# Kernel tuning notes

Hardware: AMD Instinct MI355X
Metric: run time of the kernel (lower is better)

## Reference

```python
import jax, jax.numpy as jnp
import numpy as np

T, B, D_IN, D_H, D_OUT = 16, 8192, 512, 1024, 256


def setup_inputs() -> dict:
    key = jax.random.key(0)
    ks = jax.random.split(key, 4)
    # He-style scaled init to keep activations sane
    x = jax.random.normal(ks[0], (B, D_IN), dtype=jnp.float32)
    W1 = jax.random.normal(ks[1], (T, D_IN, D_H), dtype=jnp.float32) / np.sqrt(D_IN)
    b1 = jnp.zeros((T, D_H), dtype=jnp.float32)
    W2 = jax.random.normal(ks[2], (T, D_H, D_H), dtype=jnp.float32) / np.sqrt(D_H)
    b2 = jnp.zeros((T, D_H), dtype=jnp.float32)
    W3 = jax.random.normal(ks[3], (T, D_H, D_OUT), dtype=jnp.float32) / np.sqrt(D_H)
    b3 = jnp.zeros((T, D_OUT), dtype=jnp.float32)
    return {"x": x, "W1": W1, "b1": b1, "W2": W2, "b2": b2, "W3": W3, "b3": b3}


def reference(x, W1, b1, W2, b2, W3, b3):
    # Batched over the tree dimension t: one grouped GEMM per layer instead of
    # a Python loop over trees.
    h = jax.nn.relu(jnp.einsum('bi,tih->tbh', x, W1) + b1[:, None, :])   # [T,B,H]
    h = jax.nn.relu(jnp.einsum('tbh,thk->tbk', h, W2) + b2[:, None, :])  # [T,B,H]
    out = jnp.einsum('tbh,tho->tbo', h, W3) + b3[:, None, :]             # [T,B,O]
    return jnp.mean(out, axis=0)                                          # [B,O]
```

## Files before the change

kernel.cpp:

```cpp
#include <hip/hip_runtime.h>
#include <hip/hip_bf16.h>
#include <stdint.h>

#define T_TREES 16
#define B_ROWS  8192
#define DIN     512
#define DH      1024
#define DOUT    256

typedef unsigned short u16;
typedef __attribute__((ext_vector_type(8))) short short8;
typedef __attribute__((ext_vector_type(16))) float floatx16;

__device__ __forceinline__ u16 f2bf(float f) {
    union { float f; uint32_t u; } v; v.f = f;
    uint32_t u = v.u;
    uint32_t r = (u + 0x7fffu + ((u >> 16) & 1u)) >> 16;
    return (u16)r;
}

__device__ __forceinline__ void async_copy16(const u16* g, u16* l) {
    __builtin_amdgcn_global_load_lds(
        (const __attribute__((address_space(1))) uint32_t*)g,
        (__attribute__((address_space(3))) uint32_t*)l,
        16, 0, 0);
}

__global__ void setup_kernel(const float* __restrict__ x, u16* __restrict__ xb,
                             const float* __restrict__ b3, float* __restrict__ out) {
    if (blockIdx.x < 4096) {
        int idx = blockIdx.x * 256 + threadIdx.x;
        float4 v = ((const float4*)x)[idx];
        ushort4 o;
        o.x = f2bf(v.x); o.y = f2bf(v.y); o.z = f2bf(v.z); o.w = f2bf(v.w);
        ((ushort4*)xb)[idx] = o;
    } else {
        int idx = (blockIdx.x - 4096) * 256 + threadIdx.x;
        int o = idx & (DOUT - 1);
        float s = 0.f;
#pragma unroll
        for (int t = 0; t < T_TREES; t++) s += b3[t * DOUT + o];
        out[idx] = s * (1.f / T_TREES);
    }
}

__global__ void convert_weights_kernel(const float* __restrict__ W1, const float* __restrict__ W2,
                                       const float* __restrict__ W3,
                                       u16* __restrict__ W1b, u16* __restrict__ W2b,
                                       u16* __restrict__ W3b) {
    __shared__ float tile[32][33];
    int t = blockIdx.z, tl = blockIdx.x;
    const float* in; u16* out; int K, N, kt, nt; float scale = 1.f;
    if (tl < 512)       { in = W1; out = W1b; K = DIN; N = DH;   kt = tl & 15; nt = tl >> 4; }
    else if (tl < 1536) { tl -= 512;  in = W2; out = W2b; K = DH; N = DH;   kt = tl & 31; nt = tl >> 5; }
    else                { tl -= 1536; in = W3; out = W3b; K = DH; N = DOUT; kt = tl & 31; nt = tl >> 5;
                          scale = 1.f / T_TREES; }
    int k0 = kt * 32, n0 = nt * 32;
    const float* inb = in + (size_t)t * K * N;
    u16* outb = out + (size_t)t * K * N;
    int c = threadIdx.x & 31, rg = threadIdx.x >> 5;
#pragma unroll
    for (int i = 0; i < 4; i++) {
        int r = rg * 4 + i;
        tile[r][c] = inb[(size_t)(k0 + r) * N + n0 + c];
    }
    __syncthreads();
#pragma unroll
    for (int i = 0; i < 4; i++) {
        int r = rg * 4 + i;
        outb[(size_t)(n0 + r) * K + k0 + c] = f2bf(tile[c][r] * scale);
    }
}


#define GEMM_PREAMBLE()                                          \
    const int tid = threadIdx.x;                                 \
    const int wave = tid >> 6;                                   \
    const int lane = tid & 63;                                   \
    const int l31 = lane & 31;                                   \
    const int h = lane >> 5;                                     \
    const int rb = l31 & 3;            \
    const int wm = (wave >> 1) * 64;                             \
    const int wn = (wave & 1) * 64;                              \
    const int s = lane >> 3;           \
    const int c8 = lane & 7;                                     \
    const int colElem = ((c8 ^ ((s & 3) << 1)) << 3);

#define GEMM_KSLAB(Ab, Bb, K)                                                         \
    {                                                                                  \
        _Pragma("unroll")                                                              \
        for (int i = 0; i < 4; i++) {                                                  \
            const int j = wave * 4 + i;                                                \
            const int r = j * 8 + s;                                                   \
            async_copy16(Ab + (size_t)(m0 + r) * K + kk + colElem, &ldsA[j * 512]);    \
            async_copy16(Bb + (size_t)(n0 + r) * K + kk + colElem, &ldsB[j * 512]);    \
        }                                                                              \
        __syncthreads();                                                               \
        _Pragma("unroll")                                                              \
        for (int kq = 0; kq < 4; kq++) {                                               \
            const int col = ((kq ^ rb) << 4) + h * 8;                                  \
            short8 a[2], b[2];                                                         \
            _Pragma("unroll")                                                          \
            for (int fi = 0; fi < 2; fi++)                                             \
                a[fi] = *(const short8*)&ldsA[(wm + fi * 32 + l31) * 64 + col];        \
            _Pragma("unroll")                                                          \
            for (int fj = 0; fj < 2; fj++)                                             \
                b[fj] = *(const short8*)&ldsB[(wn + fj * 32 + l31) * 64 + col];        \
            _Pragma("unroll")                                                          \
            for (int fi = 0; fi < 2; fi++)                                             \
                _Pragma("unroll")                                                      \
                for (int fj = 0; fj < 2; fj++)                                         \
                    acc[fi][fj] = __builtin_amdgcn_mfma_f32_32x32x16_bf16(             \
                        a[fi], b[fj], acc[fi][fj], 0, 0, 0);                           \
        }                                                                              \
        __syncthreads();                                                               \
    }

__global__ __launch_bounds__(256, 2)
void gemm_relu_bf16(const u16* __restrict__ A, size_t aStrideT,
                    const u16* __restrict__ Bt,
                    const float* __restrict__ bias,
                    u16* __restrict__ C,
                    int M, int N, int K) {
    __shared__ u16 ldsA[128 * 64];
    __shared__ u16 ldsB[128 * 64];

    const int t = blockIdx.z;
    const u16* Ab = A + (size_t)t * aStrideT;
    const u16* Bb = Bt + (size_t)t * (size_t)N * K;
    u16* Cb = C + (size_t)t * (size_t)M * N;
    const float* biasb = bias + (size_t)t * N;

    const int m0 = blockIdx.x * 128;
    const int n0 = blockIdx.y * 128;

    GEMM_PREAMBLE();

    floatx16 acc[2][2];
#pragma unroll
    for (int fi = 0; fi < 2; fi++)
#pragma unroll
        for (int fj = 0; fj < 2; fj++)
#pragma unroll
            for (int r = 0; r < 16; r++) acc[fi][fj][r] = 0.f;

    for (int kk = 0; kk < K; kk += 64) GEMM_KSLAB(Ab, Bb, K);

#pragma unroll
    for (int fj = 0; fj < 2; fj++) {
        const int n = n0 + wn + fj * 32 + l31;
        const float bv = biasb[n];
#pragma unroll
        for (int fi = 0; fi < 2; fi++) {
#pragma unroll
            for (int r = 0; r < 16; r++) {
                const int m = m0 + wm + fi * 32 + (r & 3) + 8 * (r >> 2) + 4 * h;
                float v = acc[fi][fj][r] + bv;
                v = v > 0.f ? v : 0.f;
                Cb[(size_t)m * N + n] = f2bf(v);
            }
        }
    }
}

__global__ __launch_bounds__(256, 2)
void gemm_final(const u16* __restrict__ H2, const u16* __restrict__ W3t,
                float* __restrict__ Out) {
    constexpr int M = B_ROWS, N = DOUT, K = DH;
    __shared__ u16 ldsA[128 * 64];
    __shared__ u16 ldsB[128 * 64];

    const int m0 = blockIdx.x * 128;
    const int n0 = blockIdx.y * 128;
    const int t = blockIdx.z;
    const u16* Ab = H2 + (size_t)t * M * K;
    const u16* Bb = W3t + (size_t)t * N * K;

    GEMM_PREAMBLE();

    floatx16 acc[2][2];
#pragma unroll
    for (int fi = 0; fi < 2; fi++)
#pragma unroll
        for (int fj = 0; fj < 2; fj++)
#pragma unroll
            for (int r = 0; r < 16; r++) acc[fi][fj][r] = 0.f;

    for (int kk = 0; kk < K; kk += 64) GEMM_KSLAB(Ab, Bb, K);

#pragma unroll
    for (int fj = 0; fj < 2; fj++) {
        const int n = n0 + wn + fj * 32 + l31;
#pragma unroll
        for (int fi = 0; fi < 2; fi++) {
#pragma unroll
            for (int r = 0; r < 16; r++) {
                const int m = m0 + wm + fi * 32 + (r & 3) + 8 * (r >> 2) + 4 * h;
                atomicAdd(&Out[(size_t)m * N + n], acc[fi][fj][r]);
            }
        }
    }
}

extern "C" void kernel_launch(void* const* d_in, const int* in_sizes, int n_in,
                              void* d_out, int out_size, void* d_ws, size_t ws_size,
                              hipStream_t stream) {
    const float* x  = (const float*)d_in[0];
    const float* W1 = (const float*)d_in[1];
    const float* b1 = (const float*)d_in[2];
    const float* W2 = (const float*)d_in[3];
    const float* b2 = (const float*)d_in[4];
    const float* W3 = (const float*)d_in[5];
    const float* b3 = (const float*)d_in[6];
    float* out = (float*)d_out;

    const size_t XB_BYTES = 8388608ull;
    const size_t W1B_BYTES = 16777216ull, W2B_BYTES = 33554432ull, W3B_BYTES = 8388608ull;
    const size_t FIXED = XB_BYTES + W1B_BYTES + W2B_BYTES + W3B_BYTES;
    const size_t PER_TREE = 33554432ull;

    uint8_t* ws = (uint8_t*)d_ws;
    u16* xb  = (u16*)ws;
    u16* W1b = (u16*)(ws + XB_BYTES);
    u16* W2b = (u16*)(ws + XB_BYTES + W1B_BYTES);
    u16* W3b = (u16*)(ws + XB_BYTES + W1B_BYTES + W2B_BYTES);
    u16* h1  = (u16*)(ws + FIXED);

    int g = 16;
    while (g > 1 && FIXED + (size_t)g * PER_TREE > ws_size) g >>= 1;
    const int nG = T_TREES / g;
    u16* h2 = (u16*)(ws + FIXED + (size_t)g * (PER_TREE / 2));

    setup_kernel<<<4096 + 8192, 256, 0, stream>>>(x, xb, b3, out);
    convert_weights_kernel<<<dim3(1792, 1, T_TREES), 256, 0, stream>>>(
        W1, W2, W3, W1b, W2b, W3b);

    for (int gi = 0; gi < nG; gi++) {
        const int t0 = gi * g;
        gemm_relu_bf16<<<dim3(B_ROWS / 128, DH / 128, g), 256, 0, stream>>>(
            xb, 0, W1b + (size_t)t0 * DIN * DH, b1 + (size_t)t0 * DH, h1, B_ROWS, DH, DIN);
        gemm_relu_bf16<<<dim3(B_ROWS / 128, DH / 128, g), 256, 0, stream>>>(
            h1, (size_t)B_ROWS * DH, W2b + (size_t)t0 * DH * DH, b2 + (size_t)t0 * DH, h2, B_ROWS, DH, DH);
        gemm_final<<<dim3(B_ROWS / 128, DOUT / 128, g), 256, 0, stream>>>(
            h2, W3b + (size_t)t0 * DH * DOUT, out);
    }
}
```

Measured before the change: 879.2 us.

## Replace final-layer atomics with per-tree partial buffers plus reduce kernel

```diff
diff --git a/kernel.cpp b/kernel.cpp
--- a/kernel.cpp
+++ b/kernel.cpp
@@ -26,50 +26,60 @@
         16, 0, 0);
 }
 
-__global__ void setup_kernel(const float* __restrict__ x, u16* __restrict__ xb,
-                             const float* __restrict__ b3, float* __restrict__ out) {
+__global__ void prep_kernel(const float* __restrict__ x, u16* __restrict__ xb,
+                            const float* __restrict__ b3, float* __restrict__ out,
+                            const float* __restrict__ W1, const float* __restrict__ W2,
+                            const float* __restrict__ W3,
+                            u16* __restrict__ W1b, u16* __restrict__ W2b,
+                            u16* __restrict__ W3b) {
+    __shared__ float tile[32][33];
     if (blockIdx.x < 4096) {
         int idx = blockIdx.x * 256 + threadIdx.x;
         float4 v = ((const float4*)x)[idx];
         ushort4 o;
         o.x = f2bf(v.x); o.y = f2bf(v.y); o.z = f2bf(v.z); o.w = f2bf(v.w);
         ((ushort4*)xb)[idx] = o;
-    } else {
+    } else if (blockIdx.x < 12288) {
         int idx = (blockIdx.x - 4096) * 256 + threadIdx.x;
         int o = idx & (DOUT - 1);
         float s = 0.f;
 #pragma unroll
         for (int t = 0; t < T_TREES; t++) s += b3[t * DOUT + o];
         out[idx] = s * (1.f / T_TREES);
-    }
-}
-
-__global__ void convert_weights_kernel(const float* __restrict__ W1, const float* __restrict__ W2,
-                                       const float* __restrict__ W3,
-                                       u16* __restrict__ W1b, u16* __restrict__ W2b,
-                                       u16* __restrict__ W3b) {
-    __shared__ float tile[32][33];
-    int t = blockIdx.z, tl = blockIdx.x;
-    const float* in; u16* out; int K, N, kt, nt; float scale = 1.f;
-    if (tl < 512)       { in = W1; out = W1b; K = DIN; N = DH;   kt = tl & 15; nt = tl >> 4; }
-    else if (tl < 1536) { tl -= 512;  in = W2; out = W2b; K = DH; N = DH;   kt = tl & 31; nt = tl >> 5; }
-    else                { tl -= 1536; in = W3; out = W3b; K = DH; N = DOUT; kt = tl & 31; nt = tl >> 5;
-                          scale = 1.f / T_TREES; }
-    int k0 = kt * 32, n0 = nt * 32;
-    const float* inb = in + (size_t)t * K * N;
-    u16* outb = out + (size_t)t * K * N;
-    int c = threadIdx.x & 31, rg = threadIdx.x >> 5;
-#pragma unroll
-    for (int i = 0; i < 4; i++) {
-        int r = rg * 4 + i;
-        tile[r][c] = inb[(size_t)(k0 + r) * N + n0 + c];
-    }
-    __syncthreads();
-#pragma unroll
-    for (int i = 0; i < 4; i++) {
-        int r = rg * 4 + i;
-        outb[(size_t)(n0 + r) * K + k0 + c] = f2bf(tile[c][r] * scale);
-    }
+    } else {
+        int bid = blockIdx.x - 12288;
+        int t = bid / 1792, tl = bid - t * 1792;
+        const float* in; u16* outp; int K, N, kt, nt; float scale = 1.f;
+        if (tl < 512)       { in = W1; outp = W1b; K = DIN; N = DH;   kt = tl & 15; nt = tl >> 4; }
+        else if (tl < 1536) { tl -= 512;  in = W2; outp = W2b; K = DH; N = DH;   kt = tl & 31; nt = tl >> 5; }
+        else                { tl -= 1536; in = W3; outp = W3b; K = DH; N = DOUT; kt = tl & 31; nt = tl >> 5;
+                              scale = 1.f / T_TREES; }
+        int k0 = kt * 32, n0 = nt * 32;
+        const float* inb = in + (size_t)t * K * N;
+        u16* outb = outp + (size_t)t * K * N;
+        int c = threadIdx.x & 31, rg = threadIdx.x >> 5;
+#pragma unroll
+        for (int i = 0; i < 4; i++) {
+            int r = rg * 4 + i;
+            tile[r][c] = inb[(size_t)(k0 + r) * N + n0 + c];
+        }
+        __syncthreads();
+#pragma unroll
+        for (int i = 0; i < 4; i++) {
+            int r = rg * 4 + i;
+            outb[(size_t)(n0 + r) * K + k0 + c] = f2bf(tile[c][r] * scale);
+        }
+    }
+}
+
+__global__ void reduce_kernel(const float* __restrict__ Part, float* __restrict__ Out, int g) {
+    int idx = blockIdx.x * 256 + threadIdx.x;
+    float4 s = ((const float4*)Out)[idx];
+    for (int t = 0; t < g; t++) {
+        float4 p = ((const float4*)(Part + (size_t)t * B_ROWS * DOUT))[idx];
+        s.x += p.x; s.y += p.y; s.z += p.z; s.w += p.w;
+    }
+    ((float4*)Out)[idx] = s;
 }
 
 
@@ -79,10 +89,10 @@
     const int lane = tid & 63;                                   \
     const int l31 = lane & 31;                                   \
     const int h = lane >> 5;                                     \
-    const int rb = l31 & 3;            \
+    const int rb = l31 & 3;                                      \
     const int wm = (wave >> 1) * 64;                             \
     const int wn = (wave & 1) * 64;                              \
-    const int s = lane >> 3;           \
+    const int s = lane >> 3;                                     \
     const int c8 = lane & 7;                                     \
     const int colElem = ((c8 ^ ((s & 3) << 1)) << 3);
 
@@ -164,8 +174,8 @@
 }
 
 __global__ __launch_bounds__(256, 2)
-void gemm_final(const u16* __restrict__ H2, const u16* __restrict__ W3t,
-                float* __restrict__ Out) {
+void gemm_final_part(const u16* __restrict__ H2, const u16* __restrict__ W3t,
+                     float* __restrict__ Part) {
     constexpr int M = B_ROWS, N = DOUT, K = DH;
     __shared__ u16 ldsA[128 * 64];
     __shared__ u16 ldsB[128 * 64];
@@ -175,6 +185,7 @@
     const int t = blockIdx.z;
     const u16* Ab = H2 + (size_t)t * M * K;
     const u16* Bb = W3t + (size_t)t * N * K;
+    float* Pb = Part + (size_t)t * M * N;
 
     GEMM_PREAMBLE();
 
@@ -196,7 +207,7 @@
 #pragma unroll
             for (int r = 0; r < 16; r++) {
                 const int m = m0 + wm + fi * 32 + (r & 3) + 8 * (r >> 2) + 4 * h;
-                atomicAdd(&Out[(size_t)m * N + n], acc[fi][fj][r]);
+                Pb[(size_t)m * N + n] = acc[fi][fj][r];
             }
         }
     }
@@ -225,15 +236,15 @@
     u16* W2b = (u16*)(ws + XB_BYTES + W1B_BYTES);
     u16* W3b = (u16*)(ws + XB_BYTES + W1B_BYTES + W2B_BYTES);
     u16* h1  = (u16*)(ws + FIXED);
+    float* part = (float*)(ws + FIXED);
 
     int g = 16;
     while (g > 1 && FIXED + (size_t)g * PER_TREE > ws_size) g >>= 1;
     const int nG = T_TREES / g;
     u16* h2 = (u16*)(ws + FIXED + (size_t)g * (PER_TREE / 2));
 
-    setup_kernel<<<4096 + 8192, 256, 0, stream>>>(x, xb, b3, out);
-    convert_weights_kernel<<<dim3(1792, 1, T_TREES), 256, 0, stream>>>(
-        W1, W2, W3, W1b, W2b, W3b);
+    prep_kernel<<<12288 + 1792 * T_TREES, 256, 0, stream>>>(
+        x, xb, b3, out, W1, W2, W3, W1b, W2b, W3b);
 
     for (int gi = 0; gi < nG; gi++) {
         const int t0 = gi * g;
@@ -241,7 +252,8 @@
             xb, 0, W1b + (size_t)t0 * DIN * DH, b1 + (size_t)t0 * DH, h1, B_ROWS, DH, DIN);
         gemm_relu_bf16<<<dim3(B_ROWS / 128, DH / 128, g), 256, 0, stream>>>(
             h1, (size_t)B_ROWS * DH, W2b + (size_t)t0 * DH * DH, b2 + (size_t)t0 * DH, h2, B_ROWS, DH, DH);
-        gemm_final<<<dim3(B_ROWS / 128, DOUT / 128, g), 256, 0, stream>>>(
-            h2, W3b + (size_t)t0 * DH * DOUT, out);
-    }
-}
+        gemm_final_part<<<dim3(B_ROWS / 128, DOUT / 128, g), 256, 0, stream>>>(
+            h2, W3b + (size_t)t0 * DH * DOUT, part);
+        reduce_kernel<<<(B_ROWS * DOUT / 4) / 256, 256, 0, stream>>>(part, out, g);
+    }
+}
```

New measurement: 820.6 us. -6.7%, faster.
